# Optimization experiments

Hardware: AMD Instinct MI355X
Metric: run time of the kernel (lower is better)

## Reference

```python
import jax, jax.numpy as jnp
import numpy as np

NUM_HEADS = 12
EPS = 1e-6


def setup_inputs() -> dict:
    key = jax.random.key(0)
    k1, k2, k3, k4, k5 = jax.random.split(key, 5)
    B, N, C = 8, 4096, 768
    scale = 1.0 / np.sqrt(C)
    return {
        "x": jax.random.normal(k1, (B, N, C), dtype=jnp.float32),
        "W_qkv": jax.random.normal(k2, (C, 3 * C), dtype=jnp.float32) * scale,
        "b_qkv": jax.random.normal(k3, (3 * C,), dtype=jnp.float32) * 0.02,
        "W_proj": jax.random.normal(k4, (C, C), dtype=jnp.float32) * scale,
        "b_proj": jax.random.normal(k5, (C,), dtype=jnp.float32) * 0.02,
    }


def reference(x, W_qkv, b_qkv, W_proj, b_proj):
    B, N, C = x.shape
    H = NUM_HEADS
    D = C // H
    # qkv projection -> (3, B, H, N, D)
    qkv = (x @ W_qkv + b_qkv).reshape(B, N, 3, H, D).transpose(2, 0, 3, 1, 4)
    q, k, v = qkv[0], qkv[1], qkv[2]
    q = jax.nn.sigmoid(q)
    k = jax.nn.sigmoid(k)
    ksum = k.sum(axis=2)  # [B,H,D]
    qsum = q.sum(axis=2)  # [B,H,D]
    # incoming/outgoing flow normalizers, [B,H,N]
    sink_incoming = 1.0 / (jnp.einsum('bhnd,bhd->bhn', q + EPS, ksum + EPS) + EPS)
    source_outgoing = 1.0 / (jnp.einsum('bhnd,bhd->bhn', k + EPS, qsum + EPS) + EPS)
    conserved_sink = jnp.einsum(
        'bhnd,bhd->bhn', q + EPS, (k * source_outgoing[..., None]).sum(axis=2) + EPS) + EPS
    conserved_source = jnp.einsum(
        'bhnd,bhd->bhn', k + EPS, (q * sink_incoming[..., None]).sum(axis=2) + EPS) + EPS
    conserved_source = jnp.clip(conserved_source, -1.0, 1.0)
    sink_allocation = jax.nn.sigmoid(conserved_sink * (float(N) / float(N)))
    source_competition = jax.nn.softmax(conserved_source, axis=-1) * float(N)
    # linear attention: kv = k^T @ (v * competition), [B,H,D,D]
    kv = jnp.einsum('bhnd,bhne->bhde', k, v * source_competition[..., None])
    x_update = jnp.einsum('bhnd,bhde->bhne', q, kv)
    x_update = x_update * sink_incoming[..., None] * sink_allocation[..., None]
    out = x_update.transpose(0, 2, 1, 3).reshape(B, N, C)
    out = out @ W_proj + b_proj
    return jax.nn.sigmoid(2.0 * out)
```

## Files before the change

### kernel.cpp

```cpp
#include <hip/hip_runtime.h>
#include <stdint.h>

#define EPSF 1e-6f

typedef unsigned short u16;
typedef __attribute__((ext_vector_type(8))) short short8;
typedef __attribute__((ext_vector_type(4))) float f32x4;

__device__ __forceinline__ float us2f(u16 u) {
  union { float f; unsigned int i; } c; c.i = ((unsigned int)u) << 16; return c.f;
}
__device__ __forceinline__ u16 f2bfu(float f) {
  union { float f; unsigned int i; } c; c.f = f;
  unsigned int i = c.i;
  return (u16)((i + 0x7FFFu + ((i >> 16) & 1u)) >> 16);
}
__device__ __forceinline__ float sigm(float x) { return 1.f / (1.f + __expf(-x)); }

typedef __attribute__((address_space(3))) unsigned int lds_u32;
typedef const __attribute__((address_space(1))) unsigned int glb_u32;
__device__ __forceinline__ void gl_lds16(const u16* g, u16* l) {
  __builtin_amdgcn_global_load_lds((glb_u32*)g, (lds_u32*)l, 16, 0, 0);
}

__global__ void k_prep(const float* __restrict__ x, u16* __restrict__ xbf,
                       const float* __restrict__ Wqkv, u16* __restrict__ WqT,
                       const float* __restrict__ Wproj, u16* __restrict__ WpT) {
  __shared__ float tile[32][33];
  const int b = blockIdx.x;
  if (b < 24576) {
    const int i = b * 256 + threadIdx.x;
    float4 v = ((const float4*)x)[i];
    ushort4 o;
    o.x = f2bfu(v.x); o.y = f2bfu(v.y); o.z = f2bfu(v.z); o.w = f2bfu(v.w);
    ((ushort4*)xbf)[i] = o;
    return;
  }
  const float* in; u16* out; int R, C, bx, by;
  if (b < 24576 + 1728) {
    const int id = b - 24576; in = Wqkv; out = WqT; R = 768; C = 2304; bx = id % 72; by = id / 72;
  } else {
    const int id = b - 26304; in = Wproj; out = WpT; R = 768; C = 768; bx = id % 24; by = id / 24;
  }
  const int tx = threadIdx.x & 31, ty = threadIdx.x >> 5;
  const int c0 = bx << 5, r0 = by << 5;
  for (int i = ty; i < 32; i += 8) tile[i][tx] = in[(size_t)(r0 + i) * C + c0 + tx];
  __syncthreads();
  for (int i = ty; i < 32; i += 8) out[(size_t)(c0 + i) * R + r0 + tx] = f2bfu(tile[tx][i]);
}

template <int MODE>
__global__ __launch_bounds__(512, 1) void k_gemm(
    const u16* __restrict__ A, const u16* __restrict__ BT,
    const float* __restrict__ bias,
    u16* __restrict__ qkvo, float* __restrict__ qsum, float* __restrict__ ksum,
    float* __restrict__ outf)
{
  __shared__ __align__(16) u16 smem[57344];
  const int tid = threadIdx.x;
  const int lane = tid & 63;
  const int wid = tid >> 6;
  const int wm = wid >> 2, wn = wid & 3;
  const int nx = gridDim.x;
  int lid = blockIdx.y * nx + blockIdx.x;
  const int q8 = (nx * gridDim.y) >> 3;
  lid = (lid & 7) * q8 + (lid >> 3);
  const int m0 = (lid / nx) << 8;
  const int n0 = (lid % nx) * 192;

  const int rowL0 = tid >> 3;
  const int gc = (tid & 7) ^ (rowL0 & 7);
  const u16* gA = A  + (size_t)(m0 + rowL0) * 768 + (gc << 3);
  const u16* gB = BT + (size_t)(n0 + rowL0) * 768 + (gc << 3);

  const int r16 = lane & 15;
  const int sgrp = lane >> 4;
  const int xk = r16 & 7;
  const int coff0 = ((sgrp) ^ xk) << 3;
  const int coff1 = ((4 + sgrp) ^ xk) << 3;
  int offB[3];
#pragma unroll
  for (int nj = 0; nj < 3; ++nj) {
    const int ub = wn * 48 + (nj << 4);
    offB[nj] = ((ub >> 6) << 12) + (((ub & 63) + r16) << 6);
  }

  f32x4 acc[8][3];
#pragma unroll
  for (int i = 0; i < 8; ++i)
#pragma unroll
    for (int j = 0; j < 3; ++j) acc[i][j] = (f32x4){0.f, 0.f, 0.f, 0.f};

#define STAGEA(tt, y)                                                         \
  do {                                                                        \
    u16* dst = &smem[(((tt) & 1) * 28672) + ((y) << 13) + (tid << 3)];        \
    const u16* s = gA + (size_t)(y) * 98304 + (tt) * 64;                      \
    gl_lds16(s, dst);                                                         \
    gl_lds16(s + 49152, dst + 4096);                                          \
  } while (0)

#define STAGEB(tt, u)                                                         \
  do {                                                                        \
    u16* dst = &smem[(((tt) & 1) * 28672) + 16384 + ((u) << 12) + (tid << 3)];\
    gl_lds16(gB + (size_t)(u) * 49152 + (tt) * 64, dst);                      \
  } while (0)

#define RDA(mi, co) (*(const short8*)(pa + ((((mi) << 4) + r16) << 6) + (co)))
#define RDB(nj, co) (*(const short8*)(pb + offB[nj] + (co)))

#define MFMA12(P, A00, A01, A10, A11)                                                               \
  do {                                                                                              \
    acc[2*(P)  ][0] = __builtin_amdgcn_mfma_f32_16x16x32_bf16(A00, bf[0][0], acc[2*(P)  ][0],0,0,0);\
    acc[2*(P)  ][1] = __builtin_amdgcn_mfma_f32_16x16x32_bf16(A00, bf[1][0], acc[2*(P)  ][1],0,0,0);\
    acc[2*(P)  ][2] = __builtin_amdgcn_mfma_f32_16x16x32_bf16(A00, bf[2][0], acc[2*(P)  ][2],0,0,0);\
    acc[2*(P)+1][0] = __builtin_amdgcn_mfma_f32_16x16x32_bf16(A10, bf[0][0], acc[2*(P)+1][0],0,0,0);\
    acc[2*(P)+1][1] = __builtin_amdgcn_mfma_f32_16x16x32_bf16(A10, bf[1][0], acc[2*(P)+1][1],0,0,0);\
    acc[2*(P)+1][2] = __builtin_amdgcn_mfma_f32_16x16x32_bf16(A10, bf[2][0], acc[2*(P)+1][2],0,0,0);\
    acc[2*(P)  ][0] = __builtin_amdgcn_mfma_f32_16x16x32_bf16(A01, bf[0][1], acc[2*(P)  ][0],0,0,0);\
    acc[2*(P)  ][1] = __builtin_amdgcn_mfma_f32_16x16x32_bf16(A01, bf[1][1], acc[2*(P)  ][1],0,0,0);\
    acc[2*(P)  ][2] = __builtin_amdgcn_mfma_f32_16x16x32_bf16(A01, bf[2][1], acc[2*(P)  ][2],0,0,0);\
    acc[2*(P)+1][0] = __builtin_amdgcn_mfma_f32_16x16x32_bf16(A11, bf[0][1], acc[2*(P)+1][0],0,0,0);\
    acc[2*(P)+1][1] = __builtin_amdgcn_mfma_f32_16x16x32_bf16(A11, bf[1][1], acc[2*(P)+1][1],0,0,0);\
    acc[2*(P)+1][2] = __builtin_amdgcn_mfma_f32_16x16x32_bf16(A11, bf[2][1], acc[2*(P)+1][2],0,0,0);\
  } while (0)

#define PH_SYNC_PRE()                                          \
    __builtin_amdgcn_s_barrier();                              \
    asm volatile("s_waitcnt lgkmcnt(0)" ::: "memory");         \
    __builtin_amdgcn_sched_barrier(0);                         \
    __builtin_amdgcn_s_setprio(1)

#define PH_SYNC_POST()                                         \
    __builtin_amdgcn_s_setprio(0);                             \
    __builtin_amdgcn_sched_barrier(0);                         \
    __builtin_amdgcn_s_barrier()

  STAGEA(0, 0); STAGEA(0, 1); STAGEB(0, 0); STAGEB(0, 1); STAGEB(0, 2);
  asm volatile("s_waitcnt vmcnt(0)" ::: "memory");
  __builtin_amdgcn_s_barrier();

  for (int t = 0; t < 12; ++t) {
    const u16* pa = &smem[(t & 1) * 28672 + (wm << 13)];
    const u16* pb = &smem[(t & 1) * 28672 + 16384];
    short8 bf[3][2];
    bf[0][0] = RDB(0, coff0); bf[0][1] = RDB(0, coff1);
    bf[1][0] = RDB(1, coff0); bf[1][1] = RDB(1, coff1);
    bf[2][0] = RDB(2, coff0); bf[2][1] = RDB(2, coff1);
    short8 a00 = RDA(0, coff0), a01 = RDA(0, coff1);
    short8 a10 = RDA(1, coff0), a11 = RDA(1, coff1);
    if (t < 11) { STAGEA(t + 1, 0); STAGEA(t + 1, 1); }
    PH_SYNC_PRE();
    MFMA12(0, a00, a01, a10, a11);
    PH_SYNC_POST();
    a00 = RDA(2, coff0); a01 = RDA(2, coff1);
    a10 = RDA(3, coff0); a11 = RDA(3, coff1);
    if (t < 11) { STAGEB(t + 1, 0); STAGEB(t + 1, 1); STAGEB(t + 1, 2); }
    PH_SYNC_PRE();
    MFMA12(1, a00, a01, a10, a11);
    PH_SYNC_POST();
    a00 = RDA(4, coff0); a01 = RDA(4, coff1);
    a10 = RDA(5, coff0); a11 = RDA(5, coff1);
    PH_SYNC_PRE();
    MFMA12(2, a00, a01, a10, a11);
    PH_SYNC_POST();
    a00 = RDA(6, coff0); a01 = RDA(6, coff1);
    a10 = RDA(7, coff0); a11 = RDA(7, coff1);
    PH_SYNC_PRE();
    MFMA12(3, a00, a01, a10, a11);
    __builtin_amdgcn_s_setprio(0);
    __builtin_amdgcn_sched_barrier(0);
    asm volatile("s_waitcnt vmcnt(0)" ::: "memory");
    __builtin_amdgcn_s_barrier();
  }
#undef PH_SYNC_PRE
#undef PH_SYNC_POST
#undef MFMA12
#undef RDA
#undef RDB
#undef STAGEA
#undef STAGEB

  if (MODE == 0) {
    const bool sg = (n0 < 1536);
    const int colc = n0 + wn * 48;
    float jsum[3] = {0.f, 0.f, 0.f};
#pragma unroll
    for (int mi = 0; mi < 8; ++mi) {
      const int rowb = m0 + (wm << 7) + (mi << 4) + ((lane >> 4) << 2);
#pragma unroll
      for (int nj = 0; nj < 3; ++nj) {
        const int col = colc + (nj << 4) + r16;
        const float bcol = bias[col];
        if (sg) {
#pragma unroll
          for (int rg = 0; rg < 4; ++rg) {
            const float val = sigm(acc[mi][nj][rg] + bcol);
            jsum[nj] += val;
            qkvo[(size_t)(rowb + rg) * 2304 + col] = f2bfu(val);
          }
        } else {
#pragma unroll
          for (int rg = 0; rg < 4; ++rg)
            qkvo[(size_t)(rowb + rg) * 2304 + col] = f2bfu(acc[mi][nj][rg] + bcol);
        }
      }
    }
    if (sg) {
#pragma unroll
      for (int nj = 0; nj < 3; ++nj) {
        jsum[nj] += __shfl_xor(jsum[nj], 16, 64);
        jsum[nj] += __shfl_xor(jsum[nj], 32, 64);
      }
      if (lane < 16) {
        const int b768 = (m0 >> 12) * 768;
        float* sdst = (n0 >= 768) ? ksum : qsum;
        const int cb = colc - ((n0 >= 768) ? 768 : 0);
#pragma unroll
        for (int nj = 0; nj < 3; ++nj)
          atomicAdd(&sdst[b768 + cb + (nj << 4) + r16], jsum[nj]);
      }
    }
  } else {
#pragma unroll
    for (int mi = 0; mi < 8; ++mi) {
      const int rowb = m0 + (wm << 7) + (mi << 4) + ((lane >> 4) << 2);
#pragma unroll
      for (int nj = 0; nj < 3; ++nj) {
        const int col = n0 + wn * 48 + (nj << 4) + r16;
        const float bcol = bias[col];
#pragma unroll
        for (int rg = 0; rg < 4; ++rg)
          outf[(size_t)(rowb + rg) * 768 + col] = sigm(2.f * (acc[mi][nj][rg] + bcol));
      }
    }
  }
}

__global__ __launch_bounds__(256) void k_flow1(
    const u16* __restrict__ qkv,
    const float* __restrict__ qsum, const float* __restrict__ ksum,
    float* __restrict__ si_out, float* __restrict__ qsi, float* __restrict__ kso)
{
  const int bh = blockIdx.x >> 3, sp = blockIdx.x & 7;
  const int tid = threadIdx.x;
  const int grp = tid >> 3;
  const int d0 = (tid & 7) << 3;
  const u16* base = qkv + (size_t)(bh / 12) * 4096 * 2304 + (bh % 12) * 64;

  float ke[8], qe[8];
#pragma unroll
  for (int u = 0; u < 8; ++u) {
    ke[u] = ksum[(bh << 6) + d0 + u] + EPSF;
    qe[u] = qsum[(bh << 6) + d0 + u] + EPSF;
  }
  float Sk = 0.f, Sq = 0.f;
#pragma unroll
  for (int u = 0; u < 8; ++u) { Sk += ke[u]; Sq += qe[u]; }
#pragma unroll
  for (int m = 1; m < 8; m <<= 1) { Sk += __shfl_xor(Sk, m, 64); Sq += __shfl_xor(Sq, m, 64); }
  const float cK = EPSF * Sk + EPSF;
  const float cQ = EPSF * Sq + EPSF;

  float aq[8], ak[8];
#pragma unroll
  for (int u = 0; u < 8; ++u) { aq[u] = 0.f; ak[u] = 0.f; }

  const int nbase = sp << 9;
  for (int it = 0; it < 16; ++it) {
    const int n = nbase + (it << 5) + grp;
    const u16* rp = base + (size_t)n * 2304 + d0;
    short8 q8 = *(const short8*)(rp);
    short8 k8 = *(const short8*)(rp + 768);
    float dq = 0.f, dk = 0.f;
#pragma unroll
    for (int u = 0; u < 8; ++u) {
      dq += us2f((u16)q8[u]) * ke[u];
      dk += us2f((u16)k8[u]) * qe[u];
    }
#pragma unroll
    for (int m = 1; m < 8; m <<= 1) { dq += __shfl_xor(dq, m, 64); dk += __shfl_xor(dk, m, 64); }
    const float si = 1.f / (dq + cK);
    const float so = 1.f / (dk + cQ);
    if ((tid & 7) == 0) si_out[(bh << 12) + n] = si;
#pragma unroll
    for (int u = 0; u < 8; ++u) {
      aq[u] += us2f((u16)q8[u]) * si;
      ak[u] += us2f((u16)k8[u]) * so;
    }
  }
  __shared__ float redq[32][68];
  __shared__ float redk[32][68];
#pragma unroll
  for (int u = 0; u < 8; ++u) { redq[grp][d0 + u] = aq[u]; redk[grp][d0 + u] = ak[u]; }
  __syncthreads();
  if (tid < 128) {
    const int which = tid >> 6, d = tid & 63;
    float s = 0.f;
    if (which == 0) {
#pragma unroll
      for (int g = 0; g < 32; ++g) s += redq[g][d];
      atomicAdd(&qsi[(bh << 6) + d], s);
    } else {
#pragma unroll
      for (int g = 0; g < 32; ++g) s += redk[g][d];
      atomicAdd(&kso[(bh << 6) + d], s);
    }
  }
}

__global__ __launch_bounds__(256) void k_fkv(
    const u16* __restrict__ qkv,
    const float* __restrict__ qsi,
    float* __restrict__ sumexp, float* __restrict__ kvm)
{
  __shared__ __align__(16) u16 smem[2 * 64 * 136];
  u16* kT = smem;
  u16* vT = smem + 64 * 136;
  const int tid = threadIdx.x;
  const int bh = blockIdx.x >> 3, sp = blockIdx.x & 7;
  const int lane = tid & 63, wid = tid >> 6;
  const int r16 = lane & 15, g = lane >> 4;
  const u16* base = qkv + (size_t)(bh / 12) * 4096 * 2304 + (bh % 12) * 64;

  const int d0 = (tid & 7) << 3;
  float qie[8];
#pragma unroll
  for (int u = 0; u < 8; ++u) qie[u] = qsi[(bh << 6) + d0 + u] + EPSF;
  float Sq = qsi[(bh << 6) + lane] + EPSF;
#pragma unroll
  for (int m = 1; m < 64; m <<= 1) Sq += __shfl_xor(Sq, m, 64);
  const float cR = EPSF * Sq + EPSF;

  f32x4 acc[4][4];
#pragma unroll
  for (int i = 0; i < 4; ++i)
#pragma unroll
    for (int j = 0; j < 4; ++j) acc[i][j] = (f32x4){0.f, 0.f, 0.f, 0.f};

  const int nf = (wid << 5) + (g << 3);
  float esum = 0.f;

  for (int st = 0; st < 4; ++st) {
    const int nst = (sp << 9) + (st << 7);
#pragma unroll
    for (int i = 0; i < 4; ++i) {
      const int c = tid + (i << 8);
      const int nl = c >> 3;
      const int ng = nst + nl;
      const u16* rp = base + (size_t)ng * 2304 + d0;
      short8 k8 = *(const short8*)(rp + 768);
      short8 v8 = *(const short8*)(rp + 1536);
      float pcr = 0.f;
#pragma unroll
      for (int u = 0; u < 8; ++u) pcr += us2f((u16)k8[u]) * qie[u];
#pragma unroll
      for (int m = 1; m < 8; m <<= 1) pcr += __shfl_xor(pcr, m, 64);
      float cr = pcr + cR;
      cr = fminf(1.f, fmaxf(-1.f, cr));
      const float ev = __expf(cr);
      const int col = nl ^ (d0 & 56);
#pragma unroll
      for (int u = 0; u < 8; ++u) {
        kT[(d0 + u) * 136 + col] = f2bfu(us2f((u16)k8[u]) * ev);
        vT[(d0 + u) * 136 + col] = (u16)(unsigned short)v8[u];
      }
      if ((tid & 7) == 0) esum += ev;
    }
    __syncthreads();

    short8 af[4], bf[4];
#pragma unroll
    for (int mi = 0; mi < 4; ++mi) {
      const int row = (mi << 4) + r16;
      af[mi] = *(const short8*)&kT[row * 136 + (nf ^ (row & 56))];
    }
#pragma unroll
    for (int nj = 0; nj < 4; ++nj) {
      const int row = (nj << 4) + r16;
      bf[nj] = *(const short8*)&vT[row * 136 + (nf ^ (row & 56))];
    }
#pragma unroll
    for (int mi = 0; mi < 4; ++mi)
#pragma unroll
      for (int nj = 0; nj < 4; ++nj)
        acc[mi][nj] = __builtin_amdgcn_mfma_f32_16x16x32_bf16(af[mi], bf[nj], acc[mi][nj], 0, 0, 0);
    __syncthreads();
  }

  float* red = (float*)smem;
  float* kvb = kvm + ((size_t)bh << 12);
#pragma unroll
  for (int half = 0; half < 2; ++half) {
#pragma unroll
    for (int m2 = 0; m2 < 2; ++m2) {
      const int mi = (half << 1) + m2;
#pragma unroll
      for (int nj = 0; nj < 4; ++nj)
#pragma unroll
        for (int rg = 0; rg < 4; ++rg)
          red[(wid << 11) + (((m2 << 4) + (g << 2) + rg) << 6) + (nj << 4) + r16] = acc[mi][nj][rg];
    }
    __syncthreads();
    const int base2 = tid << 3;
#pragma unroll
    for (int u2 = 0; u2 < 2; ++u2) {
      const int o = base2 + (u2 << 2);
      float4 s0 = *(const float4*)&red[o];
      float4 s1 = *(const float4*)&red[2048 + o];
      float4 s2 = *(const float4*)&red[4096 + o];
      float4 s3 = *(const float4*)&red[6144 + o];
      s0.x += s1.x + s2.x + s3.x;
      s0.y += s1.y + s2.y + s3.y;
      s0.z += s1.z + s2.z + s3.z;
      s0.w += s1.w + s2.w + s3.w;
      const int gi = (half << 11) + o;
      atomicAdd(&kvb[gi + 0], s0.x);
      atomicAdd(&kvb[gi + 1], s0.y);
      atomicAdd(&kvb[gi + 2], s0.z);
      atomicAdd(&kvb[gi + 3], s0.w);
    }
    __syncthreads();
  }

  esum += __shfl_xor(esum, 8, 64);
  esum += __shfl_xor(esum, 16, 64);
  esum += __shfl_xor(esum, 32, 64);
  if (lane == 0) atomicAdd(&sumexp[bh], esum);
}

__global__ __launch_bounds__(256) void k_xup(
    const u16* __restrict__ qkv, const float* __restrict__ kvm,
    const float* __restrict__ si_arr, const float* __restrict__ kso,
    const float* __restrict__ sumexp,
    u16* __restrict__ attn)
{
  const int bh = blockIdx.y;
  const int n0 = blockIdx.x << 7;
  const int b = bh / 12, h = bh % 12;
  __shared__ __align__(16) u16 qs[128 * 72];
  __shared__ __align__(16) u16 kvs[64 * 72];
  __shared__ float m_lds[128];
  const int tid = threadIdx.x, lane = tid & 63, wid = tid >> 6;
  const int d0c = (tid & 7) << 3;

  float soe[8];
#pragma unroll
  for (int u = 0; u < 8; ++u) soe[u] = kso[(bh << 6) + d0c + u] + EPSF;
  float Ss = 0.f;
#pragma unroll
  for (int u = 0; u < 8; ++u) Ss += soe[u];
#pragma unroll
  for (int m = 1; m < 8; m <<= 1) Ss += __shfl_xor(Ss, m, 64);
  const float cS = EPSF * Ss + EPSF;

  const u16* qg = qkv + (size_t)b * 4096 * 2304 + (size_t)n0 * 2304 + h * 64;
#pragma unroll
  for (int i = 0; i < 4; ++i) {
    const int c = tid + (i << 8);
    const int nl = c >> 3, d0 = (c & 7) << 3;
    short8 q8 = *(const short8*)(qg + (size_t)nl * 2304 + d0);
    *(short8*)&qs[nl * 72 + d0] = q8;
    float pcs = 0.f;
#pragma unroll
    for (int u = 0; u < 8; ++u) pcs += us2f((u16)q8[u]) * soe[u];
#pragma unroll
    for (int m = 1; m < 8; m <<= 1) pcs += __shfl_xor(pcs, m, 64);
    if ((tid & 7) == 0)
      m_lds[nl] = si_arr[((size_t)bh << 12) + n0 + nl] * sigm(pcs + cS);
  }
  const float* kvg = kvm + ((size_t)bh << 12);
#pragma unroll
  for (int i = 0; i < 4; ++i) {
    const int idx = (tid << 2) + (i << 10);
    const int d = idx >> 6, e0 = idx & 63;
    float4 vv = *(const float4*)(kvg + idx);
    kvs[(e0 + 0) * 72 + d] = f2bfu(vv.x);
    kvs[(e0 + 1) * 72 + d] = f2bfu(vv.y);
    kvs[(e0 + 2) * 72 + d] = f2bfu(vv.z);
    kvs[(e0 + 3) * 72 + d] = f2bfu(vv.w);
  }
  __syncthreads();
  const float scale = 4096.f / sumexp[bh];
  const int r16 = lane & 15, kg8 = (lane >> 4) << 3;
  f32x4 acc[2][4];
#pragma unroll
  for (int i = 0; i < 2; ++i)
#pragma unroll
    for (int j = 0; j < 4; ++j) acc[i][j] = (f32x4){0.f, 0.f, 0.f, 0.f};
#pragma unroll
  for (int kk = 0; kk < 2; ++kk) {
    short8 af[2], bfv[4];
#pragma unroll
    for (int mi = 0; mi < 2; ++mi)
      af[mi] = *(const short8*)&qs[((wid << 5) + (mi << 4) + r16) * 72 + (kk << 5) + kg8];
#pragma unroll
    for (int nj = 0; nj < 4; ++nj)
      bfv[nj] = *(const short8*)&kvs[((nj << 4) + r16) * 72 + (kk << 5) + kg8];
#pragma unroll
    for (int mi = 0; mi < 2; ++mi)
#pragma unroll
      for (int nj = 0; nj < 4; ++nj)
        acc[mi][nj] = __builtin_amdgcn_mfma_f32_16x16x32_bf16(af[mi], bfv[nj], acc[mi][nj], 0, 0, 0);
  }
#pragma unroll
  for (int mi = 0; mi < 2; ++mi) {
#pragma unroll
    for (int rg = 0; rg < 4; ++rg) {
      const int nloc = (wid << 5) + (mi << 4) + ((lane >> 4) << 2) + rg;
      const int n = n0 + nloc;
      const float mult = m_lds[nloc] * scale;
#pragma unroll
      for (int nj = 0; nj < 4; ++nj) {
        const int e = (nj << 4) + r16;
        attn[((size_t)(b * 4096 + n)) * 768 + (h << 6) + e] = f2bfu(acc[mi][nj][rg] * mult);
      }
    }
  }
}

extern "C" void kernel_launch(void* const* d_in, const int* in_sizes, int n_in,
                              void* d_out, int out_size, void* d_ws, size_t ws_size,
                              hipStream_t stream)
{
  (void)in_sizes; (void)n_in; (void)out_size; (void)ws_size;
  const float* x     = (const float*)d_in[0];
  const float* Wqkv  = (const float*)d_in[1];
  const float* bqkv  = (const float*)d_in[2];
  const float* Wproj = (const float*)d_in[3];
  const float* bproj = (const float*)d_in[4];
  float* out = (float*)d_out;

  char* ws = (char*)d_ws;
  size_t off = 0;
  auto alloc = [&](size_t bytes) -> char* {
    char* p = ws + off;
    off += (bytes + 255) & ~(size_t)255;
    return p;
  };
  u16* qkv  = (u16*)alloc(150994944);
  u16* xbf  = (u16*)alloc(50331648);
  u16* WqT  = (u16*)alloc(3538944);
  u16* WpT  = (u16*)alloc(1179648);
  float* si = (float*)alloc(1572864);
  char* zbase = ws + off;
  float* qsum   = (float*)alloc(24576);
  float* ksum   = (float*)alloc(24576);
  float* qsi    = (float*)alloc(24576);
  float* kso    = (float*)alloc(24576);
  float* sumexp = (float*)alloc(512);
  float* kvm    = (float*)alloc(1572864);
  const size_t zbytes = (size_t)((ws + off) - zbase);

  hipMemsetAsync(zbase, 0, zbytes, stream);
  k_prep<<<26880, 256, 0, stream>>>(x, xbf, Wqkv, WqT, Wproj, WpT);
  k_gemm<0><<<dim3(12, 128), 512, 0, stream>>>(xbf, WqT, bqkv, qkv, qsum, ksum, nullptr);
  k_flow1<<<768, 256, 0, stream>>>(qkv, qsum, ksum, si, qsi, kso);
  k_fkv<<<768, 256, 0, stream>>>(qkv, qsi, sumexp, kvm);
  k_xup<<<dim3(32, 96), 256, 0, stream>>>(qkv, kvm, si, kso, sumexp, xbf);
  k_gemm<1><<<dim3(4, 128), 512, 0, stream>>>(xbf, WpT, bproj, nullptr, nullptr, nullptr, out);
}
```

Before: 374.7 us.

## Halve GEMM K-tile to 32 so two workgroups fit per CU

The GEMM main loop now stages a K-tile of 32 instead of 64, which halves the LDS footprint of the double buffer. Launch bounds are raised to allow two 512-thread workgroups per CU. The LDS swizzle and the per-lane offsets are rebuilt for 64-byte rows, and the loop runs 24 iterations with two MFMA phases instead of 12 iterations with four. The aim is more latency hiding through higher occupancy, at the cost of twice as many barriers and waits per K and tighter register limits that may cause spills with 96 accumulator floats.

```diff
diff --git a/kernel.cpp b/kernel.cpp
--- a/kernel.cpp
+++ b/kernel.cpp
@@ -50,13 +50,13 @@
 }
 
 template <int MODE>
-__global__ __launch_bounds__(512, 1) void k_gemm(
+__global__ __launch_bounds__(512, 2) void k_gemm(
     const u16* __restrict__ A, const u16* __restrict__ BT,
     const float* __restrict__ bias,
     u16* __restrict__ qkvo, float* __restrict__ qsum, float* __restrict__ ksum,
     float* __restrict__ outf)
 {
-  __shared__ __align__(16) u16 smem[57344];
+  __shared__ __align__(16) u16 smem[28672];
   const int tid = threadIdx.x;
   const int lane = tid & 63;
   const int wid = tid >> 6;
@@ -68,22 +68,21 @@
   const int m0 = (lid / nx) << 8;
   const int n0 = (lid % nx) * 192;
 
-  const int rowL0 = tid >> 3;
-  const int gc = (tid & 7) ^ (rowL0 & 7);
-  const u16* gA = A  + (size_t)(m0 + rowL0) * 768 + (gc << 3);
-  const u16* gB = BT + (size_t)(n0 + rowL0) * 768 + (gc << 3);
+  const int rowA = tid >> 2;
+  const int gcA = (tid & 3) ^ ((rowA >> 1) & 3);
+  const u16* gA = A + (size_t)(m0 + rowA) * 768 + (gcA << 3);
+  const int rowB = tid >> 2;
+  const int gcB = (tid & 3) ^ ((rowB >> 1) & 3);
+  const u16* gB = BT + (size_t)(n0 + rowB) * 768 + (gcB << 3);
 
   const int r16 = lane & 15;
   const int sgrp = lane >> 4;
-  const int xk = r16 & 7;
-  const int coff0 = ((sgrp) ^ xk) << 3;
-  const int coff1 = ((4 + sgrp) ^ xk) << 3;
-  int offB[3];
-#pragma unroll
-  for (int nj = 0; nj < 3; ++nj) {
-    const int ub = wn * 48 + (nj << 4);
-    offB[nj] = ((ub >> 6) << 12) + (((ub & 63) + r16) << 6);
-  }
+  const int coff = ((sgrp ^ ((r16 >> 1) & 3)) << 3);
+  int offA[8], offB[3];
+#pragma unroll
+  for (int mi = 0; mi < 8; ++mi) offA[mi] = ((wm << 7) + (mi << 4) + r16) * 32 + coff;
+#pragma unroll
+  for (int nj = 0; nj < 3; ++nj) offB[nj] = (wn * 48 + (nj << 4) + r16) * 32 + coff;
 
   f32x4 acc[8][3];
 #pragma unroll
@@ -91,37 +90,35 @@
 #pragma unroll
     for (int j = 0; j < 3; ++j) acc[i][j] = (f32x4){0.f, 0.f, 0.f, 0.f};
 
-#define STAGEA(tt, y)                                                         \
-  do {                                                                        \
-    u16* dst = &smem[(((tt) & 1) * 28672) + ((y) << 13) + (tid << 3)];        \
-    const u16* s = gA + (size_t)(y) * 98304 + (tt) * 64;                      \
-    gl_lds16(s, dst);                                                         \
-    gl_lds16(s + 49152, dst + 4096);                                          \
+#define ABASE(tt) (((tt) & 1) * 14336)
+#define BBASE(tt) (ABASE(tt) + 8192)
+#define STAGEA(tt)                                                    \
+  do {                                                                \
+    u16* d = &smem[ABASE(tt) + (tid << 3)];                           \
+    gl_lds16(gA + (tt) * 32, d);                                      \
+    gl_lds16(gA + 98304 + (tt) * 32, d + 4096);                      \
   } while (0)
-
-#define STAGEB(tt, u)                                                         \
-  do {                                                                        \
-    u16* dst = &smem[(((tt) & 1) * 28672) + 16384 + ((u) << 12) + (tid << 3)];\
-    gl_lds16(gB + (size_t)(u) * 49152 + (tt) * 64, dst);                      \
+#define STAGEB(tt)                                                    \
+  do {                                                                \
+    gl_lds16(gB + (tt) * 32, &smem[BBASE(tt) + (tid << 3)]);          \
+    if (tid < 256)                                                    \
+      gl_lds16(gB + 98304 + (tt) * 32, &smem[BBASE(tt) + 4096 + (tid << 3)]); \
   } while (0)
 
-#define RDA(mi, co) (*(const short8*)(pa + ((((mi) << 4) + r16) << 6) + (co)))
-#define RDB(nj, co) (*(const short8*)(pb + offB[nj] + (co)))
-
-#define MFMA12(P, A00, A01, A10, A11)                                                               \
-  do {                                                                                              \
-    acc[2*(P)  ][0] = __builtin_amdgcn_mfma_f32_16x16x32_bf16(A00, bf[0][0], acc[2*(P)  ][0],0,0,0);\
-    acc[2*(P)  ][1] = __builtin_amdgcn_mfma_f32_16x16x32_bf16(A00, bf[1][0], acc[2*(P)  ][1],0,0,0);\
-    acc[2*(P)  ][2] = __builtin_amdgcn_mfma_f32_16x16x32_bf16(A00, bf[2][0], acc[2*(P)  ][2],0,0,0);\
-    acc[2*(P)+1][0] = __builtin_amdgcn_mfma_f32_16x16x32_bf16(A10, bf[0][0], acc[2*(P)+1][0],0,0,0);\
-    acc[2*(P)+1][1] = __builtin_amdgcn_mfma_f32_16x16x32_bf16(A10, bf[1][0], acc[2*(P)+1][1],0,0,0);\
-    acc[2*(P)+1][2] = __builtin_amdgcn_mfma_f32_16x16x32_bf16(A10, bf[2][0], acc[2*(P)+1][2],0,0,0);\
-    acc[2*(P)  ][0] = __builtin_amdgcn_mfma_f32_16x16x32_bf16(A01, bf[0][1], acc[2*(P)  ][0],0,0,0);\
-    acc[2*(P)  ][1] = __builtin_amdgcn_mfma_f32_16x16x32_bf16(A01, bf[1][1], acc[2*(P)  ][1],0,0,0);\
-    acc[2*(P)  ][2] = __builtin_amdgcn_mfma_f32_16x16x32_bf16(A01, bf[2][1], acc[2*(P)  ][2],0,0,0);\
-    acc[2*(P)+1][0] = __builtin_amdgcn_mfma_f32_16x16x32_bf16(A11, bf[0][1], acc[2*(P)+1][0],0,0,0);\
-    acc[2*(P)+1][1] = __builtin_amdgcn_mfma_f32_16x16x32_bf16(A11, bf[1][1], acc[2*(P)+1][1],0,0,0);\
-    acc[2*(P)+1][2] = __builtin_amdgcn_mfma_f32_16x16x32_bf16(A11, bf[2][1], acc[2*(P)+1][2],0,0,0);\
+#define MFMA12(MB, A0, A1, A2, A3)                                                              \
+  do {                                                                                          \
+    acc[(MB)  ][0] = __builtin_amdgcn_mfma_f32_16x16x32_bf16(A0, b0, acc[(MB)  ][0], 0, 0, 0);  \
+    acc[(MB)  ][1] = __builtin_amdgcn_mfma_f32_16x16x32_bf16(A0, b1, acc[(MB)  ][1], 0, 0, 0);  \
+    acc[(MB)  ][2] = __builtin_amdgcn_mfma_f32_16x16x32_bf16(A0, b2, acc[(MB)  ][2], 0, 0, 0);  \
+    acc[(MB)+1][0] = __builtin_amdgcn_mfma_f32_16x16x32_bf16(A1, b0, acc[(MB)+1][0], 0, 0, 0);  \
+    acc[(MB)+1][1] = __builtin_amdgcn_mfma_f32_16x16x32_bf16(A1, b1, acc[(MB)+1][1], 0, 0, 0);  \
+    acc[(MB)+1][2] = __builtin_amdgcn_mfma_f32_16x16x32_bf16(A1, b2, acc[(MB)+1][2], 0, 0, 0);  \
+    acc[(MB)+2][0] = __builtin_amdgcn_mfma_f32_16x16x32_bf16(A2, b0, acc[(MB)+2][0], 0, 0, 0);  \
+    acc[(MB)+2][1] = __builtin_amdgcn_mfma_f32_16x16x32_bf16(A2, b1, acc[(MB)+2][1], 0, 0, 0);  \
+    acc[(MB)+2][2] = __builtin_amdgcn_mfma_f32_16x16x32_bf16(A2, b2, acc[(MB)+2][2], 0, 0, 0);  \
+    acc[(MB)+3][0] = __builtin_amdgcn_mfma_f32_16x16x32_bf16(A3, b0, acc[(MB)+3][0], 0, 0, 0);  \
+    acc[(MB)+3][1] = __builtin_amdgcn_mfma_f32_16x16x32_bf16(A3, b1, acc[(MB)+3][1], 0, 0, 0);  \
+    acc[(MB)+3][2] = __builtin_amdgcn_mfma_f32_16x16x32_bf16(A3, b2, acc[(MB)+3][2], 0, 0, 0);  \
   } while (0)
 
 #define PH_SYNC_PRE()                                          \
@@ -135,38 +132,31 @@
     __builtin_amdgcn_sched_barrier(0);                         \
     __builtin_amdgcn_s_barrier()
 
-  STAGEA(0, 0); STAGEA(0, 1); STAGEB(0, 0); STAGEB(0, 1); STAGEB(0, 2);
+  STAGEA(0); STAGEB(0);
   asm volatile("s_waitcnt vmcnt(0)" ::: "memory");
   __builtin_amdgcn_s_barrier();
 
-  for (int t = 0; t < 12; ++t) {
-    const u16* pa = &smem[(t & 1) * 28672 + (wm << 13)];
-    const u16* pb = &smem[(t & 1) * 28672 + 16384];
-    short8 bf[3][2];
-    bf[0][0] = RDB(0, coff0); bf[0][1] = RDB(0, coff1);
-    bf[1][0] = RDB(1, coff0); bf[1][1] = RDB(1, coff1);
-    bf[2][0] = RDB(2, coff0); bf[2][1] = RDB(2, coff1);
-    short8 a00 = RDA(0, coff0), a01 = RDA(0, coff1);
-    short8 a10 = RDA(1, coff0), a11 = RDA(1, coff1);
-    if (t < 11) { STAGEA(t + 1, 0); STAGEA(t + 1, 1); }
+  for (int t = 0; t < 24; ++t) {
+    const u16* pa = &smem[ABASE(t)];
+    const u16* pb = &smem[BBASE(t)];
+    short8 b0 = *(const short8*)(pb + offB[0]);
+    short8 b1 = *(const short8*)(pb + offB[1]);
+    short8 b2 = *(const short8*)(pb + offB[2]);
+    short8 a0 = *(const short8*)(pa + offA[0]);
+    short8 a1 = *(const short8*)(pa + offA[1]);
+    short8 a2 = *(const short8*)(pa + offA[2]);
+    short8 a3 = *(const short8*)(pa + offA[3]);
+    if (t < 23) STAGEA(t + 1);
     PH_SYNC_PRE();
-    MFMA12(0, a00, a01, a10, a11);
+    MFMA12(0, a0, a1, a2, a3);
     PH_SYNC_POST();
-    a00 = RDA(2, coff0); a01 = RDA(2, coff1);
-    a10 = RDA(3, coff0); a11 = RDA(3, coff1);
-    if (t < 11) { STAGEB(t + 1, 0); STAGEB(t + 1, 1); STAGEB(t + 1, 2); }
+    a0 = *(const short8*)(pa + offA[4]);
+    a1 = *(const short8*)(pa + offA[5]);
+    a2 = *(const short8*)(pa + offA[6]);
+    a3 = *(const short8*)(pa + offA[7]);
+    if (t < 23) STAGEB(t + 1);
     PH_SYNC_PRE();
-    MFMA12(1, a00, a01, a10, a11);
-    PH_SYNC_POST();
-    a00 = RDA(4, coff0); a01 = RDA(4, coff1);
-    a10 = RDA(5, coff0); a11 = RDA(5, coff1);
-    PH_SYNC_PRE();
-    MFMA12(2, a00, a01, a10, a11);
-    PH_SYNC_POST();
-    a00 = RDA(6, coff0); a01 = RDA(6, coff1);
-    a10 = RDA(7, coff0); a11 = RDA(7, coff1);
-    PH_SYNC_PRE();
-    MFMA12(3, a00, a01, a10, a11);
+    MFMA12(4, a0, a1, a2, a3);
     __builtin_amdgcn_s_setprio(0);
     __builtin_amdgcn_sched_barrier(0);
     asm volatile("s_waitcnt vmcnt(0)" ::: "memory");
@@ -175,10 +165,10 @@
 #undef PH_SYNC_PRE
 #undef PH_SYNC_POST
 #undef MFMA12
-#undef RDA
-#undef RDB
 #undef STAGEA
 #undef STAGEB
+#undef ABASE
+#undef BBASE
 
   if (MODE == 0) {
     const bool sg = (n0 < 1536);
```

Measured after the change: 384.0 us. 2.5% more time.
